# Performance work log

Hardware: AMD Instinct MI355X
Metric: run time of the kernel (lower is better)

Reference implementation:

```python
import jax, jax.numpy as jnp
import numpy as np

ROUTING_ITERS = 3


def _squash(x, axis=-1):
    # sum_sq/(1+sum_sq) * x/sqrt(sum_sq), faithful to the torch squash
    sum_sq = jnp.sum(x * x, axis=axis, keepdims=True)
    return sum_sq / (1.0 + sum_sq) * x / jnp.sqrt(sum_sq)


def setup_inputs() -> dict:
    key = jax.random.key(0)
    k1, k2 = jax.random.split(key)
    B, I, O, Din, Dout = 256, 1152, 10, 8, 16
    x = jax.random.normal(k1, (B, I, Din), dtype=jnp.float32)
    W = jax.random.normal(k2, (I, O, Din, Dout), dtype=jnp.float32)
    return {"x": x, "W": W}


def reference(x, W):
    # x: [B, I, Din], W: [I, O, Din, Dout]
    I, O, Din, Dout = W.shape
    # u_hat = x @ W per (capsule_in, capsule_out): [B, I, O, Dout]
    u_hat = jnp.einsum('bid,iode->bioe', x, W)
    b = jnp.zeros((I, O), dtype=x.dtype)  # coupling logits, shared over batch
    v = None
    for _ in range(ROUTING_ITERS):
        c = jax.nn.softmax(b, axis=1)                    # softmax over out capsules
        s = jnp.einsum('bioe,io->boe', u_hat, c)         # weighted sum over in caps
        v = _squash(s, axis=-1)                          # [B, O, Dout]
        # agreement, averaged over batch (torch does .mean(dim=0))
        agree = jnp.einsum('bioe,boe->bio', u_hat, v).mean(axis=0)  # [I, O]
        b = b + agree
    # torch returns v.squeeze(1).transpose(2,3) -> [B, O, Dout, 1]
    return v[..., None]
```

## Files before the change

### kernel.cpp

```cpp
#include <hip/hip_runtime.h>
#include <math.h>

#define B    256
#define I    1152
#define O    10
#define DIN  8
#define DOUT 16
#define OE   160
#define XROW 9216
#define WROW 1280
#define PSPLIT 72
#define CHUNK  16
#define SI     8

#define WPREP_BLOCKS ((I * OE) / 256)

typedef __attribute__((ext_vector_type(8))) short short8;
typedef __attribute__((ext_vector_type(4))) float floatx4;

__device__ __forceinline__ unsigned short f2bf(float f) {
    unsigned u = __builtin_bit_cast(unsigned, f);
    u += 0x7fffu + ((u >> 16) & 1u);
    return (unsigned short)(u >> 16);
}
__device__ __forceinline__ float bf2f(unsigned short h) {
    unsigned u = ((unsigned)h) << 16;
    return __builtin_bit_cast(float, u);
}

__device__ __forceinline__ void split8(const float* __restrict__ xp,
                                       short8& h8, short8& l8)
{
    float4 v0 = *(const float4*)xp;
    float4 v1 = *(const float4*)(xp + 4);
    float v[8] = {v0.x, v0.y, v0.z, v0.w, v1.x, v1.y, v1.z, v1.w};
#pragma unroll
    for (int d = 0; d < 8; ++d) {
        unsigned short h = f2bf(v[d]);
        h8[d] = (short)h;
        l8[d] = (short)f2bf(v[d] - bf2f(h));
    }
}

__global__ __launch_bounds__(256) void wprep_kernel(
    const float* __restrict__ W, float* __restrict__ Wt)
{
    int g  = blockIdx.x * 256 + threadIdx.x;
    int i  = g / OE;
    int oe = g - i * OE;
    int o  = oe >> 4;
    int e  = oe & 15;
    const float* wp = W + (size_t)i * WROW + o * (DIN * DOUT) + e;
    float4 a, b;
    a.x = wp[0 * DOUT]; a.y = wp[1 * DOUT]; a.z = wp[2 * DOUT]; a.w = wp[3 * DOUT];
    b.x = wp[4 * DOUT]; b.y = wp[5 * DOUT]; b.z = wp[6 * DOUT]; b.w = wp[7 * DOUT];
    float4* dst = (float4*)(Wt + (size_t)g * 8);
    dst[0] = a;
    dst[1] = b;
}

__global__ __launch_bounds__(256) void spart_mfma(
    const float* __restrict__ x,
    const float* __restrict__ Wt, const float* __restrict__ c,
    float* __restrict__ sp, int first)
{
    __shared__ unsigned short Wh[80 * 64], Wl[80 * 64];

    int bid = blockIdx.x;
    int ic  = bid >> 2;
    int mb  = (bid >> 1) & 1;
    int nb  = bid & 1;
    int b0  = mb * 128;
    int oe0 = nb * 80;
    int i0  = ic * CHUNK;

    int t    = threadIdx.x;
    int w    = t >> 6;
    int lane = t & 63;
    int l15  = lane & 15;
    int q    = lane >> 4;

    floatx4 acc[2][5];
#pragma unroll
    for (int mt = 0; mt < 2; ++mt)
#pragma unroll
        for (int nt = 0; nt < 5; ++nt) acc[mt][nt] = (floatx4)(0.f);

#pragma unroll
    for (int round = 0; round < CHUNK / SI; ++round) {
        int si0 = i0 + round * SI;
        if (round) __syncthreads();

        short8 ah[2][2], al[2][2];
#pragma unroll
        for (int ks = 0; ks < 2; ++ks)
#pragma unroll
            for (int mt = 0; mt < 2; ++mt) {
                const float* xp = x + (size_t)(b0 + w * 32 + mt * 16 + l15) * XROW
                                + (size_t)si0 * 8 + (ks << 5) + (q << 3);
                split8(xp, ah[ks][mt], al[ks][mt]);
            }

#pragma unroll
        for (int r = 0; r < 3; ++r) {
            int p = t + 256 * r;
            if (p < 640) {
                int oeL = p % 80;
                int iL  = p / 80;
                int o   = (oe0 + oeL) >> 4;
                const float* wp = Wt + ((size_t)(si0 + iL) * OE + oe0 + oeL) * 8;
                float cv = first ? 0.1f : c[(si0 + iL) * O + o];
                float4 w0 = *(const float4*)wp;
                float4 w1 = *(const float4*)(wp + 4);
                float wv[8] = {w0.x, w0.y, w0.z, w0.w, w1.x, w1.y, w1.z, w1.w};
                short8 hv, lv;
#pragma unroll
                for (int d = 0; d < 8; ++d) {
                    float s = wv[d] * cv;
                    unsigned short h = f2bf(s);
                    hv[d] = (short)h;
                    lv[d] = (short)f2bf(s - bf2f(h));
                }
                int off = oeL * 64 + ((iL ^ (oeL & 7)) << 3);
                *(short8*)(Wh + off) = hv;
                *(short8*)(Wl + off) = lv;
            }
        }
        __syncthreads();

#pragma unroll
        for (int ks = 0; ks < 2; ++ks) {
#pragma unroll
            for (int nt = 0; nt < 5; ++nt) {
                int rn  = nt * 16 + l15;
                int off = rn * 64 + ((((ks << 2) + q) ^ (rn & 7)) << 3);
                short8 bh = *(const short8*)(Wh + off);
                short8 bl = *(const short8*)(Wl + off);
#pragma unroll
                for (int mt = 0; mt < 2; ++mt) {
                    acc[mt][nt] = __builtin_amdgcn_mfma_f32_16x16x32_bf16(ah[ks][mt], bh, acc[mt][nt], 0, 0, 0);
                    acc[mt][nt] = __builtin_amdgcn_mfma_f32_16x16x32_bf16(ah[ks][mt], bl, acc[mt][nt], 0, 0, 0);
                    acc[mt][nt] = __builtin_amdgcn_mfma_f32_16x16x32_bf16(al[ks][mt], bh, acc[mt][nt], 0, 0, 0);
                }
            }
        }
    }

    float* base = sp + (size_t)ic * (B * OE);
#pragma unroll
    for (int mt = 0; mt < 2; ++mt) {
        int row0 = b0 + w * 32 + mt * 16 + q * 4;
#pragma unroll
        for (int nt = 0; nt < 5; ++nt) {
            int col = oe0 + nt * 16 + l15;
#pragma unroll
            for (int reg = 0; reg < 4; ++reg)
                base[(row0 + reg) * OE + col] = acc[mt][nt][reg];
        }
    }
}

__global__ __launch_bounds__(256) void vred_kernel(
    const float* __restrict__ sp, float* __restrict__ dst)
{
    int g = blockIdx.x * 256 + threadIdx.x;
    float s = 0.f;
#pragma unroll 8
    for (int ic = 0; ic < PSPLIT; ++ic) s += sp[(size_t)ic * (B * OE) + g];

    float ss = s * s;
    ss += __shfl_xor(ss, 1, 16);
    ss += __shfl_xor(ss, 2, 16);
    ss += __shfl_xor(ss, 4, 16);
    ss += __shfl_xor(ss, 8, 16);
    float f = sqrtf(ss) / (1.f + ss);
    dst[g] = s * f;
}

__global__ __launch_bounds__(320) void agree_kernel(
    const float* __restrict__ x, const float* __restrict__ Wt,
    const float* __restrict__ v, float* __restrict__ blog,
    float* __restrict__ c, int first)
{
    int i  = blockIdx.x;
    int t  = threadIdx.x;
    int dg = (t >= OE) ? 1 : 0;
    int oe = t - dg * OE;

    __shared__ float4 Xl[B][2];
    __shared__ float  G[DIN * OE];
    __shared__ float  brow[O];

#pragma unroll
    for (int k = 0; k < 2; ++k) {
        int idx = t + 320 * k;
        if (idx < 512) {
            int r = idx >> 1;
            int h = idx & 1;
            Xl[r][h] = *(const float4*)(x + (size_t)r * XROW + i * DIN + h * 4);
        }
    }
    __syncthreads();

    float a0 = 0.f, a1 = 0.f, a2 = 0.f, a3 = 0.f;
    const float* vp = v + oe;
#pragma unroll 8
    for (int bb = 0; bb < B; ++bb) {
        float  vv = vp[bb * OE];
        float4 xq = Xl[bb][dg];
        a0 = fmaf(xq.x, vv, a0);
        a1 = fmaf(xq.y, vv, a1);
        a2 = fmaf(xq.z, vv, a2);
        a3 = fmaf(xq.w, vv, a3);
    }

    int d0 = dg * 4;
    G[(d0 + 0) * OE + oe] = a0;
    G[(d0 + 1) * OE + oe] = a1;
    G[(d0 + 2) * OE + oe] = a2;
    G[(d0 + 3) * OE + oe] = a3;
    __syncthreads();

    if (t < OE) {
        int o = t >> 4;
        const float* wr = Wt + ((size_t)i * OE + t) * 8;
        float4 wa = *(const float4*)wr;
        float4 wb = *(const float4*)(wr + 4);
        float p = 0.f;
        p = fmaf(wa.x, G[0 * OE + t], p);
        p = fmaf(wa.y, G[1 * OE + t], p);
        p = fmaf(wa.z, G[2 * OE + t], p);
        p = fmaf(wa.w, G[3 * OE + t], p);
        p = fmaf(wb.x, G[4 * OE + t], p);
        p = fmaf(wb.y, G[5 * OE + t], p);
        p = fmaf(wb.z, G[6 * OE + t], p);
        p = fmaf(wb.w, G[7 * OE + t], p);
        p += __shfl_xor(p, 8, 16);
        p += __shfl_xor(p, 4, 16);
        p += __shfl_xor(p, 2, 16);
        p += __shfl_xor(p, 1, 16);
        if ((t & 15) == 0) {
            float bo = first ? 0.f : blog[i * O + o];
            bo += p * (1.f / (float)B);
            blog[i * O + o] = bo;
            brow[o] = bo;
        }
    }
    __syncthreads();

    if (t == 0) {
        float m = brow[0];
#pragma unroll
        for (int o = 1; o < O; ++o) m = fmaxf(m, brow[o]);
        float ex[O];
        float sum = 0.f;
#pragma unroll
        for (int o = 0; o < O; ++o) { ex[o] = __expf(brow[o] - m); sum += ex[o]; }
        float inv = 1.f / sum;
#pragma unroll
        for (int o = 0; o < O; ++o) c[i * O + o] = ex[o] * inv;
    }
}

extern "C" void kernel_launch(void* const* d_in, const int* in_sizes, int n_in,
                              void* d_out, int out_size, void* d_ws, size_t ws_size,
                              hipStream_t stream)
{
    const float* x = (const float*)d_in[0];
    const float* W = (const float*)d_in[1];
    float* out = (float*)d_out;

    float* blog = (float*)d_ws;
    float* cbuf = blog + I * O;
    float* vbuf = cbuf + I * O;
    float* Wt   = vbuf + B * OE;
    float* sp   = Wt + (size_t)I * OE * DIN;

    wprep_kernel<<<WPREP_BLOCKS, 256, 0, stream>>>(W, Wt);

    dim3 gs(4 * PSPLIT), bs(256);
    spart_mfma<<<gs, bs, 0, stream>>>(x, Wt, cbuf, sp, 1);
    vred_kernel<<<160, 256, 0, stream>>>(sp, vbuf);
    agree_kernel<<<I, 320, 0, stream>>>(x, Wt, vbuf, blog, cbuf, 1);
    spart_mfma<<<gs, bs, 0, stream>>>(x, Wt, cbuf, sp, 0);
    vred_kernel<<<160, 256, 0, stream>>>(sp, vbuf);
    agree_kernel<<<I, 320, 0, stream>>>(x, Wt, vbuf, blog, cbuf, 0);
    spart_mfma<<<gs, bs, 0, stream>>>(x, Wt, cbuf, sp, 0);
    vred_kernel<<<160, 256, 0, stream>>>(sp, out);
}
```

Baseline: 159.7 us.

## Replace scalar agreement kernel with split-bf16 MFMA GEMM and fuse softmax into spart

The per-capsule scalar agree kernel is replaced by a GEMM over the batch, G = xT·v, using split-bf16 MFMA. Its inputs are x pre-transposed and split into hi/lo bf16 in a prep kernel, and v stored transposed as hi/lo by vred. The W·G reduction, logit update and softmax now run at the start of each spart_mfma block, which removes the separate coupling buffer. This cuts redundant scalar FMA work over the batch. In exchange it adds a large G buffer write/read, an x transpose pass, and redundant logit computation across the four blocks sharing an input chunk.

```diff
diff --git a/kernel.cpp b/kernel.cpp
--- a/kernel.cpp
+++ b/kernel.cpp
@@ -13,7 +13,9 @@
 #define CHUNK  16
 #define SI     8
 
-#define WPREP_BLOCKS ((I * OE) / 256)
+#define WPREP_BLOCKS 720
+#define XT_BLOCKS    1152
+#define PREP_BLOCKS  (WPREP_BLOCKS + XT_BLOCKS)
 
 typedef __attribute__((ext_vector_type(8))) short short8;
 typedef __attribute__((ext_vector_type(4))) float floatx4;
@@ -42,29 +44,56 @@
     }
 }
 
-__global__ __launch_bounds__(256) void wprep_kernel(
-    const float* __restrict__ W, float* __restrict__ Wt)
-{
-    int g  = blockIdx.x * 256 + threadIdx.x;
-    int i  = g / OE;
-    int oe = g - i * OE;
-    int o  = oe >> 4;
-    int e  = oe & 15;
-    const float* wp = W + (size_t)i * WROW + o * (DIN * DOUT) + e;
-    float4 a, b;
-    a.x = wp[0 * DOUT]; a.y = wp[1 * DOUT]; a.z = wp[2 * DOUT]; a.w = wp[3 * DOUT];
-    b.x = wp[4 * DOUT]; b.y = wp[5 * DOUT]; b.z = wp[6 * DOUT]; b.w = wp[7 * DOUT];
-    float4* dst = (float4*)(Wt + (size_t)g * 8);
-    dst[0] = a;
-    dst[1] = b;
+__global__ __launch_bounds__(256) void prep_kernel(
+    const float* __restrict__ x, const float* __restrict__ W,
+    float* __restrict__ Wt,
+    unsigned short* __restrict__ xTh, unsigned short* __restrict__ xTl)
+{
+    int blk = blockIdx.x;
+    int t   = threadIdx.x;
+    if (blk < WPREP_BLOCKS) {
+        int g  = blk * 256 + t;
+        int i  = g / OE;
+        int oe = g - i * OE;
+        int o  = oe >> 4;
+        int e  = oe & 15;
+        const float* wp = W + (size_t)i * WROW + o * (DIN * DOUT) + e;
+        float4 a, b;
+        a.x = wp[0 * DOUT]; a.y = wp[1 * DOUT]; a.z = wp[2 * DOUT]; a.w = wp[3 * DOUT];
+        b.x = wp[4 * DOUT]; b.y = wp[5 * DOUT]; b.z = wp[6 * DOUT]; b.w = wp[7 * DOUT];
+        float4* dst = (float4*)(Wt + (size_t)g * 8);
+        dst[0] = a;
+        dst[1] = b;
+    } else {
+        int g2  = blk - WPREP_BLOCKS;
+        int idb = g2 % 144;
+        int bb  = g2 / 144;
+        int id  = idb * 64 + (t & 63);
+        int b0  = bb * 32 + (t >> 6) * 8;
+        float v[8];
+#pragma unroll
+        for (int j = 0; j < 8; ++j)
+            v[j] = x[(size_t)(b0 + j) * XROW + id];
+        short8 h8, l8;
+#pragma unroll
+        for (int j = 0; j < 8; ++j) {
+            unsigned short h = f2bf(v[j]);
+            h8[j] = (short)h;
+            l8[j] = (short)f2bf(v[j] - bf2f(h));
+        }
+        *(short8*)(xTh + (size_t)id * B + b0) = h8;
+        *(short8*)(xTl + (size_t)id * B + b0) = l8;
+    }
 }
 
 __global__ __launch_bounds__(256) void spart_mfma(
-    const float* __restrict__ x,
-    const float* __restrict__ Wt, const float* __restrict__ c,
-    float* __restrict__ sp, int first)
+    const float* __restrict__ x, const float* __restrict__ Wt,
+    const float* __restrict__ G, float* __restrict__ blog,
+    float* __restrict__ sp, int phase)
 {
     __shared__ unsigned short Wh[80 * 64], Wl[80 * 64];
+    __shared__ float brow_s[16][10];
+    __shared__ float cL[16][10];
 
     int bid = blockIdx.x;
     int ic  = bid >> 2;
@@ -80,6 +109,43 @@
     int l15  = lane & 15;
     int q    = lane >> 4;
 
+    if (phase) {
+        if (t < 160) {
+            int iL = t / 10;
+            int o  = t - iL * 10;
+            int i  = i0 + iL;
+            const float4* wp = (const float4*)(Wt + (size_t)i * WROW + o * 128);
+            const float4* gp = (const float4*)(G  + (size_t)i * WROW + o * 128);
+            float sacc = 0.f;
+#pragma unroll
+            for (int j = 0; j < 32; ++j) {
+                float4 wv = wp[j], gv = gp[j];
+                sacc = fmaf(wv.x, gv.x, sacc);
+                sacc = fmaf(wv.y, gv.y, sacc);
+                sacc = fmaf(wv.z, gv.z, sacc);
+                sacc = fmaf(wv.w, gv.w, sacc);
+            }
+            float bo = sacc * (1.f / (float)B);
+            if (phase == 2) bo += blog[i * O + o];
+            else if ((bid & 3) == 0) blog[i * O + o] = bo;
+            brow_s[iL][o] = bo;
+        }
+        __syncthreads();
+        if (t < 16) {
+            float m = brow_s[t][0];
+#pragma unroll
+            for (int o = 1; o < O; ++o) m = fmaxf(m, brow_s[t][o]);
+            float ex[O];
+            float sum = 0.f;
+#pragma unroll
+            for (int o = 0; o < O; ++o) { ex[o] = __expf(brow_s[t][o] - m); sum += ex[o]; }
+            float inv = 1.f / sum;
+#pragma unroll
+            for (int o = 0; o < O; ++o) cL[t][o] = ex[o] * inv;
+        }
+        __syncthreads();
+    }
+
     floatx4 acc[2][5];
 #pragma unroll
     for (int mt = 0; mt < 2; ++mt)
@@ -109,7 +175,7 @@
                 int iL  = p / 80;
                 int o   = (oe0 + oeL) >> 4;
                 const float* wp = Wt + ((size_t)(si0 + iL) * OE + oe0 + oeL) * 8;
-                float cv = first ? 0.1f : c[(si0 + iL) * O + o];
+                float cv = phase ? cL[round * SI + iL][o] : 0.1f;
                 float4 w0 = *(const float4*)wp;
                 float4 w1 = *(const float4*)(wp + 4);
                 float wv[8] = {w0.x, w0.y, w0.z, w0.w, w1.x, w1.y, w1.z, w1.w};
@@ -161,7 +227,8 @@
 }
 
 __global__ __launch_bounds__(256) void vred_kernel(
-    const float* __restrict__ sp, float* __restrict__ dst)
+    const float* __restrict__ sp, float* __restrict__ dst,
+    unsigned short* __restrict__ vhT, unsigned short* __restrict__ vlT, int last)
 {
     int g = blockIdx.x * 256 + threadIdx.x;
     float s = 0.f;
@@ -174,91 +241,101 @@
     ss += __shfl_xor(ss, 4, 16);
     ss += __shfl_xor(ss, 8, 16);
     float f = sqrtf(ss) / (1.f + ss);
-    dst[g] = s * f;
-}
-
-__global__ __launch_bounds__(320) void agree_kernel(
-    const float* __restrict__ x, const float* __restrict__ Wt,
-    const float* __restrict__ v, float* __restrict__ blog,
-    float* __restrict__ c, int first)
-{
-    int i  = blockIdx.x;
-    int t  = threadIdx.x;
-    int dg = (t >= OE) ? 1 : 0;
-    int oe = t - dg * OE;
-
-    __shared__ float4 Xl[B][2];
-    __shared__ float  G[DIN * OE];
-    __shared__ float  brow[O];
-
-#pragma unroll
-    for (int k = 0; k < 2; ++k) {
-        int idx = t + 320 * k;
-        if (idx < 512) {
-            int r = idx >> 1;
-            int h = idx & 1;
-            Xl[r][h] = *(const float4*)(x + (size_t)r * XROW + i * DIN + h * 4);
-        }
-    }
-    __syncthreads();
-
-    float a0 = 0.f, a1 = 0.f, a2 = 0.f, a3 = 0.f;
-    const float* vp = v + oe;
-#pragma unroll 8
-    for (int bb = 0; bb < B; ++bb) {
-        float  vv = vp[bb * OE];
-        float4 xq = Xl[bb][dg];
-        a0 = fmaf(xq.x, vv, a0);
-        a1 = fmaf(xq.y, vv, a1);
-        a2 = fmaf(xq.z, vv, a2);
-        a3 = fmaf(xq.w, vv, a3);
-    }
-
-    int d0 = dg * 4;
-    G[(d0 + 0) * OE + oe] = a0;
-    G[(d0 + 1) * OE + oe] = a1;
-    G[(d0 + 2) * OE + oe] = a2;
-    G[(d0 + 3) * OE + oe] = a3;
-    __syncthreads();
-
-    if (t < OE) {
-        int o = t >> 4;
-        const float* wr = Wt + ((size_t)i * OE + t) * 8;
-        float4 wa = *(const float4*)wr;
-        float4 wb = *(const float4*)(wr + 4);
-        float p = 0.f;
-        p = fmaf(wa.x, G[0 * OE + t], p);
-        p = fmaf(wa.y, G[1 * OE + t], p);
-        p = fmaf(wa.z, G[2 * OE + t], p);
-        p = fmaf(wa.w, G[3 * OE + t], p);
-        p = fmaf(wb.x, G[4 * OE + t], p);
-        p = fmaf(wb.y, G[5 * OE + t], p);
-        p = fmaf(wb.z, G[6 * OE + t], p);
-        p = fmaf(wb.w, G[7 * OE + t], p);
-        p += __shfl_xor(p, 8, 16);
-        p += __shfl_xor(p, 4, 16);
-        p += __shfl_xor(p, 2, 16);
-        p += __shfl_xor(p, 1, 16);
-        if ((t & 15) == 0) {
-            float bo = first ? 0.f : blog[i * O + o];
-            bo += p * (1.f / (float)B);
-            blog[i * O + o] = bo;
-            brow[o] = bo;
-        }
-    }
-    __syncthreads();
-
-    if (t == 0) {
-        float m = brow[0];
-#pragma unroll
-        for (int o = 1; o < O; ++o) m = fmaxf(m, brow[o]);
-        float ex[O];
-        float sum = 0.f;
-#pragma unroll
-        for (int o = 0; o < O; ++o) { ex[o] = __expf(brow[o] - m); sum += ex[o]; }
-        float inv = 1.f / sum;
-#pragma unroll
-        for (int o = 0; o < O; ++o) c[i * O + o] = ex[o] * inv;
+    float val = s * f;
+
+    if (last) {
+        dst[g] = val;
+    } else {
+        int b  = g / OE;
+        int oe = g - b * OE;
+        unsigned short h = f2bf(val);
+        vhT[oe * B + b] = h;
+        vlT[oe * B + b] = f2bf(val - bf2f(h));
+    }
+}
+
+__global__ __launch_bounds__(256) void ggemm_kernel(
+    const unsigned short* __restrict__ xTh, const unsigned short* __restrict__ xTl,
+    const unsigned short* __restrict__ vhT, const unsigned short* __restrict__ vlT,
+    float* __restrict__ G)
+{
+    __shared__ unsigned short Vh[80 * 64], Vl[80 * 64];
+
+    int bid = blockIdx.x;
+    int m0  = (bid >> 1) * 128;
+    int nb  = bid & 1;
+    int oe0 = nb * 80;
+
+    int t    = threadIdx.x;
+    int w    = t >> 6;
+    int lane = t & 63;
+    int l15  = lane & 15;
+    int q    = lane >> 4;
+
+    floatx4 acc[2][5];
+#pragma unroll
+    for (int mt = 0; mt < 2; ++mt)
+#pragma unroll
+        for (int nt = 0; nt < 5; ++nt) acc[mt][nt] = (floatx4)(0.f);
+
+#pragma unroll
+    for (int win = 0; win < 4; ++win) {
+        int k0 = win * 64;
+        if (win) __syncthreads();
+
+#pragma unroll
+        for (int r = 0; r < 3; ++r) {
+            int p = t + 256 * r;
+            if (p < 640) {
+                int row = p >> 3;
+                int ch  = p & 7;
+                int off = row * 64 + ((ch ^ (row & 7)) << 3);
+                size_t gsrc = (size_t)(oe0 + row) * B + k0 + (ch << 3);
+                *(short8*)(Vh + off) = *(const short8*)(vhT + gsrc);
+                *(short8*)(Vl + off) = *(const short8*)(vlT + gsrc);
+            }
+        }
+        __syncthreads();
+
+        short8 ah[2][2], al[2][2];
+#pragma unroll
+        for (int ks = 0; ks < 2; ++ks)
+#pragma unroll
+            for (int mt = 0; mt < 2; ++mt) {
+                size_t ga = (size_t)(m0 + w * 32 + mt * 16 + l15) * B
+                          + k0 + (ks << 5) + (q << 3);
+                ah[ks][mt] = *(const short8*)(xTh + ga);
+                al[ks][mt] = *(const short8*)(xTl + ga);
+            }
+
+#pragma unroll
+        for (int ks = 0; ks < 2; ++ks) {
+#pragma unroll
+            for (int nt = 0; nt < 5; ++nt) {
+                int rn  = nt * 16 + l15;
+                int off = rn * 64 + ((((ks << 2) + q) ^ (rn & 7)) << 3);
+                short8 bh = *(const short8*)(Vh + off);
+                short8 bl = *(const short8*)(Vl + off);
+#pragma unroll
+                for (int mt = 0; mt < 2; ++mt) {
+                    acc[mt][nt] = __builtin_amdgcn_mfma_f32_16x16x32_bf16(ah[ks][mt], bh, acc[mt][nt], 0, 0, 0);
+                    acc[mt][nt] = __builtin_amdgcn_mfma_f32_16x16x32_bf16(ah[ks][mt], bl, acc[mt][nt], 0, 0, 0);
+                    acc[mt][nt] = __builtin_amdgcn_mfma_f32_16x16x32_bf16(al[ks][mt], bh, acc[mt][nt], 0, 0, 0);
+                }
+            }
+        }
+    }
+
+#pragma unroll
+    for (int mt = 0; mt < 2; ++mt) {
+        int rb = m0 + w * 32 + mt * 16 + q * 4;
+        int i  = rb >> 3;
+        int d0 = rb & 7;
+#pragma unroll
+        for (int nt = 0; nt < 5; ++nt) {
+            int col = oe0 + nt * 16 + l15;
+            *(floatx4*)(G + (size_t)i * WROW + col * 8 + d0) = acc[mt][nt];
+        }
     }
 }
 
@@ -271,20 +348,23 @@
     float* out = (float*)d_out;
 
     float* blog = (float*)d_ws;
-    float* cbuf = blog + I * O;
-    float* vbuf = cbuf + I * O;
-    float* Wt   = vbuf + B * OE;
-    float* sp   = Wt + (size_t)I * OE * DIN;
-
-    wprep_kernel<<<WPREP_BLOCKS, 256, 0, stream>>>(W, Wt);
+    float* Wt   = blog + I * O;
+    float* G    = Wt + (size_t)I * OE * DIN;
+    float* sp   = G  + (size_t)I * OE * DIN;
+    unsigned short* xTh = (unsigned short*)(sp + (size_t)PSPLIT * B * OE);
+    unsigned short* xTl = xTh + (size_t)XROW * B;
+    unsigned short* vhT = xTl + (size_t)XROW * B;
+    unsigned short* vlT = vhT + (size_t)B * OE;
+
+    prep_kernel<<<PREP_BLOCKS, 256, 0, stream>>>(x, W, Wt, xTh, xTl);
 
     dim3 gs(4 * PSPLIT), bs(256);
-    spart_mfma<<<gs, bs, 0, stream>>>(x, Wt, cbuf, sp, 1);
-    vred_kernel<<<160, 256, 0, stream>>>(sp, vbuf);
-    agree_kernel<<<I, 320, 0, stream>>>(x, Wt, vbuf, blog, cbuf, 1);
-    spart_mfma<<<gs, bs, 0, stream>>>(x, Wt, cbuf, sp, 0);
-    vred_kernel<<<160, 256, 0, stream>>>(sp, vbuf);
-    agree_kernel<<<I, 320, 0, stream>>>(x, Wt, vbuf, blog, cbuf, 0);
-    spart_mfma<<<gs, bs, 0, stream>>>(x, Wt, cbuf, sp, 0);
-    vred_kernel<<<160, 256, 0, stream>>>(sp, out);
-}
+    spart_mfma<<<gs, bs, 0, stream>>>(x, Wt, G, blog, sp, 0);
+    vred_kernel<<<160, 256, 0, stream>>>(sp, out, vhT, vlT, 0);
+    ggemm_kernel<<<144, 256, 0, stream>>>(xTh, xTl, vhT, vlT, G);
+    spart_mfma<<<gs, bs, 0, stream>>>(x, Wt, G, blog, sp, 1);
+    vred_kernel<<<160, 256, 0, stream>>>(sp, out, vhT, vlT, 0);
+    ggemm_kernel<<<144, 256, 0, stream>>>(xTh, xTl, vhT, vlT, G);
+    spart_mfma<<<gs, bs, 0, stream>>>(x, Wt, G, blog, sp, 2);
+    vred_kernel<<<160, 256, 0, stream>>>(sp, out, vhT, vlT, 1);
+}
```

Result: slower. 173.4 us (+8.6%).
